# Kernel optimization log

Measured on AMD Instinct MI355X. Metric: run time of the kernel, lower is better.

Reference implementation:

```python
import jax, jax.numpy as jnp
import numpy as np


def setup_inputs() -> dict:
    key = jax.random.key(0)
    k1, k2, k3 = jax.random.split(key, 3)
    T, H, HK, D = 4096, 32, 8, 128  # packed tokens, q heads, kv heads, head dim
    q = jax.random.normal(k1, (T, H, D), dtype=jnp.float32)
    k = jax.random.normal(k2, (T, HK, D), dtype=jnp.float32)
    v = jax.random.normal(k3, (T, HK, D), dtype=jnp.float32)
    return {"q": q, "k": k, "v": v, "num_seqs": 4}


def reference(q, k, v, num_seqs):
    # Varlen prefill causal attention (flash_attn_varlen_func equivalent),
    # equal-length packing: cu_seqlens = [0, S, 2S, ...].
    T, H, D = q.shape
    HK = k.shape[1]
    B = int(num_seqs)
    S = T // B
    scale = 1.0 / jnp.sqrt(jnp.asarray(D, dtype=q.dtype))
    qr = q.reshape(B, S, H, D)
    # GQA: repeat kv heads to match q heads
    rep = H // HK
    kr = jnp.repeat(k.reshape(B, S, HK, D), rep, axis=2)  # [B,S,H,D]
    vr = jnp.repeat(v.reshape(B, S, HK, D), rep, axis=2)
    scores = jnp.einsum("bqhd,bkhd->bhqk", qr, kr) * scale  # [B,H,S,S]
    causal = jnp.tril(jnp.ones((S, S), dtype=bool))
    neg = jnp.asarray(jnp.finfo(scores.dtype).min, dtype=scores.dtype)
    scores = jnp.where(causal, scores, neg)
    p = jax.nn.softmax(scores, axis=-1)
    o = jnp.einsum("bhqk,bkhd->bqhd", p, vr)  # [B,S,H,D]
    return o.reshape(T, H, D)
```

## Files before the change

kernel.cpp:

```cpp
#include <hip/hip_runtime.h>

typedef short short8 __attribute__((ext_vector_type(8)));
typedef float f32x16 __attribute__((ext_vector_type(16)));
typedef int   int4v  __attribute__((ext_vector_type(4)));
typedef int   int2v  __attribute__((ext_vector_type(2)));

#define T_TOK 4096
#define NH    32
#define NKV   8
#define HD    128
#define QREP  (NH / NKV)
#define LDS_PAIR 16384

__device__ __forceinline__ unsigned short f32_to_bf16_bits(float x) {
  union { float f; unsigned u; } a; a.f = x;
  unsigned r = a.u + 0x7fffu + ((a.u >> 16) & 1u);
  return (unsigned short)(r >> 16);
}
__device__ __forceinline__ unsigned pack_bf16(float a, float b) {
  return (unsigned)f32_to_bf16_bits(a) | ((unsigned)f32_to_bf16_bits(b) << 16);
}
__device__ __forceinline__ unsigned cvtpk(float a, float b) {
  unsigned r;
  asm("v_cvt_pk_bf16_f32 %0, %1, %2" : "=v"(r) : "v"(a), "v"(b));
  return r;
}

__device__ __forceinline__ void stage16(const unsigned short* g, unsigned short* l) {
  __builtin_amdgcn_global_load_lds(
      (const __attribute__((address_space(1))) unsigned int*)g,
      (__attribute__((address_space(3))) unsigned int*)l,
      16, 0, 0);
}

__device__ __forceinline__ short8 p_frag(const f32x16& p, int st, int hi) {
  unsigned c01 = cvtpk(p[8*st+0], p[8*st+1]);
  unsigned c23 = cvtpk(p[8*st+2], p[8*st+3]);
  unsigned c45 = cvtpk(p[8*st+4], p[8*st+5]);
  unsigned c67 = cvtpk(p[8*st+6], p[8*st+7]);
  unsigned x01 = (unsigned)__shfl_xor((int)c01, 32, 64);
  unsigned x23 = (unsigned)__shfl_xor((int)c23, 32, 64);
  unsigned x45 = (unsigned)__shfl_xor((int)c45, 32, 64);
  unsigned x67 = (unsigned)__shfl_xor((int)c67, 32, 64);
  int4v pi;
  pi[0] = (int)(hi ? x45 : c01);
  pi[1] = (int)(hi ? x67 : c23);
  pi[2] = (int)(hi ? c45 : x01);
  pi[3] = (int)(hi ? c67 : x23);
  return __builtin_bit_cast(short8, pi);
}

__global__ __launch_bounds__(256)
void pack_k(const float* __restrict__ k, unsigned short* __restrict__ kf,
            const int* __restrict__ nseq) {
  int tid  = blockIdx.x * 256 + threadIdx.x;
  int lane = tid & 63;
  int dc   = (tid >> 6) & 7;
  int gt   = (tid >> 9) & (T_TOK / 32 - 1);
  int kvh  = tid >> 16;
  int c = lane & 31, hi = lane >> 5;
  int token = gt * 32 + c;
  const float* src = k + ((size_t)token * NKV + kvh) * HD + dc * 16 + hi * 8;
  float4 a  = *reinterpret_cast<const float4*>(src);
  float4 b4 = *reinterpret_cast<const float4*>(src + 4);
  const int B = *nseq, S = T_TOK / B, S32 = S >> 5;
  int bseq = gt / S32, tile = gt - bseq * S32;
  size_t off = ((size_t)(bseq * NKV + kvh) * S32 + tile) * 4096 + dc * 512 + lane * 8;
  int4v wv; wv[0] = (int)pack_bf16(a.x, a.y);   wv[1] = (int)pack_bf16(a.z, a.w);
            wv[2] = (int)pack_bf16(b4.x, b4.y); wv[3] = (int)pack_bf16(b4.z, b4.w);
  *reinterpret_cast<int4v*>(kf + off) = wv;
}

__global__ __launch_bounds__(256)
void pack_v(const float* __restrict__ v, unsigned short* __restrict__ vf,
            const int* __restrict__ nseq) {
  int tid  = blockIdx.x * 256 + threadIdx.x;
  int lane = tid & 63;
  int idx  = (tid >> 6) & 7;
  int gt   = (tid >> 9) & (T_TOK / 32 - 1);
  int kvh  = tid >> 16;
  int c = lane & 31, hi = lane >> 5;
  int st = idx >> 2, dt = idx & 3;
  int token0 = gt * 32 + 16 * st + 8 * hi;
  const float* src = v + ((size_t)token0 * NKV + kvh) * HD + dt * 32 + c;
  unsigned u[4];
  #pragma unroll
  for (int jj = 0; jj < 4; ++jj) {
    float a = src[(size_t)(2 * jj)     * (NKV * HD)];
    float b = src[(size_t)(2 * jj + 1) * (NKV * HD)];
    u[jj] = pack_bf16(a, b);
  }
  const int B = *nseq, S = T_TOK / B, S32 = S >> 5;
  int bseq = gt / S32, tile = gt - bseq * S32;
  size_t off = ((size_t)(bseq * NKV + kvh) * S32 + tile) * 4096 + idx * 512 + lane * 8;
  int4v wv; wv[0] = (int)u[0]; wv[1] = (int)u[1]; wv[2] = (int)u[2]; wv[3] = (int)u[3];
  *reinterpret_cast<int4v*>(vf + off) = wv;
}

__global__ __launch_bounds__(256, 2)
void attn_fwd_fast(const float* __restrict__ q,
                   const unsigned short* __restrict__ kfp,
                   const unsigned short* __restrict__ vfp,
                   const int* __restrict__ nseq,
                   float* __restrict__ out)
{
  __shared__ __align__(16) unsigned short sm[2 * LDS_PAIR];

  const int bid  = blockIdx.x;
  const int h    = bid & (NH - 1);
  const int z    = bid >> 5;
  const int w    = threadIdx.x >> 6;
  const int lane = threadIdx.x & 63;
  const int c    = lane & 31;
  const int hi   = lane >> 5;

  const int B = *nseq;
  const int S = T_TOK / B;
  const int S32 = S >> 5;
  const int RBS = S >> 7;

  const int rloc = RBS - 1 - (z / B);
  const int seq  = z - (z / B) * B;
  const int rb   = seq * RBS + rloc;

  const int rbase = rb * 128;
  const int row0  = rbase + w * 32;
  const int s0    = row0 - seq * S;
  const int ntw   = s0 / 32 + 1;
  const int diag  = ntw - 1;
  const int npb   = (rloc * 4 + 4) >> 1;

  const float sl2e = 0.08838834764831845f * 1.4426950408889634f;

  const int kvh = h / QREP;
  const unsigned short* kf_blk = kfp + ((size_t)(seq * NKV + kvh) * S32) * 4096;
  const unsigned short* vf_blk = vfp + ((size_t)(seq * NKV + kvh) * S32) * 4096;
  const unsigned short* sbase = (w & 2) ? vf_blk : kf_blk;

  {
    const unsigned short* src = sbase + (size_t)(w & 1) * 4096 + lane * 8;
    unsigned short* dst = sm + w * 4096;
    #pragma unroll
    for (int j = 0; j < 8; ++j) stage16(src + j * 512, dst + j * 512);
  }

  char* qlds = (char*)(sm + LDS_PAIR);
  {
    #pragma unroll
    for (int j = 0; j < 16; ++j) {
      const int rowb = w * 32 + 2 * j + hi;
      const float* gsrc = q + ((size_t)(rbase + rowb) * NH + h) * HD + 4 * c;
      float4 a = *reinterpret_cast<const float4*>(gsrc);
      int2v u;
      u[0] = (int)cvtpk(a.x * sl2e, a.y * sl2e);
      u[1] = (int)cvtpk(a.z * sl2e, a.w * sl2e);
      const int off = (rowb * 256 + 8 * c) ^ ((rowb & 7) << 4);
      *reinterpret_cast<int2v*>(qlds + off) = u;
    }
  }
  __syncthreads();

  short8 qf[8];
  {
    const int rowb = w * 32 + c;
    #pragma unroll
    for (int dc = 0; dc < 8; ++dc) {
      const int off = (rowb * 256 + dc * 32 + hi * 16) ^ ((c & 7) << 4);
      qf[dc] = *reinterpret_cast<const short8*>(qlds + off);
    }
  }
  __syncthreads();

  f32x16 o0 = {}, o1 = {}, o2 = {}, o3 = {};
  float m = -1e30f, l = 0.0f;

  for (int i = 0; i < npb; ++i) {
    unsigned short* cur = sm + (i & 1) * LDS_PAIR;

    if (i + 1 < npb) {
      const unsigned short* src =
          sbase + (size_t)(2 * (i + 1) + (w & 1)) * 4096 + lane * 8;
      unsigned short* dst = sm + ((i + 1) & 1) * LDS_PAIR + w * 4096;
      #pragma unroll
      for (int j = 0; j < 8; ++j) stage16(src + j * 512, dst + j * 512);
    }

    if (2 * i < ntw) {
      const int ta = 2 * i, tb = 2 * i + 1;
      const unsigned short* kA = cur + lane * 8;
      const unsigned short* kB = cur + 4096 + lane * 8;
      const unsigned short* vA = cur + 8192 + lane * 8;
      const unsigned short* vB = cur + 12288 + lane * 8;

      f32x16 sa = {}, sb = {};
      #pragma unroll
      for (int dc = 0; dc < 8; ++dc) {
        short8 ka  = *reinterpret_cast<const short8*>(kA + dc * 512);
        short8 kb8 = *reinterpret_cast<const short8*>(kB + dc * 512);
        sa = __builtin_amdgcn_mfma_f32_32x32x16_bf16(ka,  qf[dc], sa, 0, 0, 0);
        sb = __builtin_amdgcn_mfma_f32_32x32x16_bf16(kb8, qf[dc], sb, 0, 0, 0);
      }

      const int qs = s0 + c;
      if (tb >= diag) {
        #pragma unroll
        for (int r = 0; r < 16; ++r) {
          int key = tb * 32 + (r & 3) + 8 * (r >> 2) + 4 * hi;
          if (key > qs) sb[r] = -1e30f;
        }
      }
      if (ta >= diag) {
        #pragma unroll
        for (int r = 0; r < 16; ++r) {
          int key = ta * 32 + (r & 3) + 8 * (r >> 2) + 4 * hi;
          if (key > qs) sa[r] = -1e30f;
        }
      }

      float pm = fmaxf(sa[0], sb[0]);
      #pragma unroll
      for (int r = 1; r < 16; ++r) pm = fmaxf(pm, fmaxf(sa[r], sb[r]));
      pm = fmaxf(pm, __shfl_xor(pm, 32));

      if (!__all(pm - m <= 8.0f)) {
        float mn = fmaxf(m, pm);
        float al = __builtin_amdgcn_exp2f(m - mn);
        m = mn;
        l *= al;
        #pragma unroll
        for (int r = 0; r < 16; ++r) {
          float ar = __shfl(al, (r & 3) + 8 * (r >> 2) + 4 * hi, 64);
          o0[r] *= ar; o1[r] *= ar; o2[r] *= ar; o3[r] *= ar;
        }
      }

      float rs = 0.0f;
      f32x16 pA, pB;
      #pragma unroll
      for (int r = 0; r < 16; ++r) {
        pA[r] = __builtin_amdgcn_exp2f(sa[r] - m);
        pB[r] = __builtin_amdgcn_exp2f(sb[r] - m);
        rs += pA[r] + pB[r];
      }
      rs += __shfl_xor(rs, 32);
      l += rs;

      short8 fa0 = p_frag(pA, 0, hi), fa1 = p_frag(pA, 1, hi);
      short8 fb0 = p_frag(pB, 0, hi), fb1 = p_frag(pB, 1, hi);

      short8 va00 = *reinterpret_cast<const short8*>(vA);
      short8 va01 = *reinterpret_cast<const short8*>(vA + 512);
      short8 va02 = *reinterpret_cast<const short8*>(vA + 1024);
      short8 va03 = *reinterpret_cast<const short8*>(vA + 1536);
      short8 va10 = *reinterpret_cast<const short8*>(vA + 2048);
      short8 va11 = *reinterpret_cast<const short8*>(vA + 2560);
      short8 va12 = *reinterpret_cast<const short8*>(vA + 3072);
      short8 va13 = *reinterpret_cast<const short8*>(vA + 3584);
      o0 = __builtin_amdgcn_mfma_f32_32x32x16_bf16(fa0, va00, o0, 0, 0, 0);
      o1 = __builtin_amdgcn_mfma_f32_32x32x16_bf16(fa0, va01, o1, 0, 0, 0);
      o2 = __builtin_amdgcn_mfma_f32_32x32x16_bf16(fa0, va02, o2, 0, 0, 0);
      o3 = __builtin_amdgcn_mfma_f32_32x32x16_bf16(fa0, va03, o3, 0, 0, 0);
      o0 = __builtin_amdgcn_mfma_f32_32x32x16_bf16(fa1, va10, o0, 0, 0, 0);
      o1 = __builtin_amdgcn_mfma_f32_32x32x16_bf16(fa1, va11, o1, 0, 0, 0);
      o2 = __builtin_amdgcn_mfma_f32_32x32x16_bf16(fa1, va12, o2, 0, 0, 0);
      o3 = __builtin_amdgcn_mfma_f32_32x32x16_bf16(fa1, va13, o3, 0, 0, 0);
      short8 vb00 = *reinterpret_cast<const short8*>(vB);
      short8 vb01 = *reinterpret_cast<const short8*>(vB + 512);
      short8 vb02 = *reinterpret_cast<const short8*>(vB + 1024);
      short8 vb03 = *reinterpret_cast<const short8*>(vB + 1536);
      short8 vb10 = *reinterpret_cast<const short8*>(vB + 2048);
      short8 vb11 = *reinterpret_cast<const short8*>(vB + 2560);
      short8 vb12 = *reinterpret_cast<const short8*>(vB + 3072);
      short8 vb13 = *reinterpret_cast<const short8*>(vB + 3584);
      o0 = __builtin_amdgcn_mfma_f32_32x32x16_bf16(fb0, vb00, o0, 0, 0, 0);
      o1 = __builtin_amdgcn_mfma_f32_32x32x16_bf16(fb0, vb01, o1, 0, 0, 0);
      o2 = __builtin_amdgcn_mfma_f32_32x32x16_bf16(fb0, vb02, o2, 0, 0, 0);
      o3 = __builtin_amdgcn_mfma_f32_32x32x16_bf16(fb0, vb03, o3, 0, 0, 0);
      o0 = __builtin_amdgcn_mfma_f32_32x32x16_bf16(fb1, vb10, o0, 0, 0, 0);
      o1 = __builtin_amdgcn_mfma_f32_32x32x16_bf16(fb1, vb11, o1, 0, 0, 0);
      o2 = __builtin_amdgcn_mfma_f32_32x32x16_bf16(fb1, vb12, o2, 0, 0, 0);
      o3 = __builtin_amdgcn_mfma_f32_32x32x16_bf16(fb1, vb13, o3, 0, 0, 0);
    }

    __syncthreads();
  }

  float linv = 1.0f / l;
  #pragma unroll
  for (int r = 0; r < 16; ++r) {
    int qp_ = (r & 3) + 8 * (r >> 2) + 4 * hi;
    float li = __shfl(linv, qp_, 64);
    float* op = out + ((size_t)(row0 + qp_) * NH + h) * HD + c;
    op[0]  = o0[r] * li;
    op[32] = o1[r] * li;
    op[64] = o2[r] * li;
    op[96] = o3[r] * li;
  }
}

__global__ __launch_bounds__(256, 2)
void attn_fwd_slow(const float* __restrict__ q,
                   const float* __restrict__ kp_,
                   const float* __restrict__ vp_,
                   const int* __restrict__ nseq,
                   float* __restrict__ out)
{
  const int bid  = blockIdx.x;
  const int h    = bid & (NH - 1);
  const int rb   = (T_TOK / 128 - 1) - (bid >> 5);
  const int kvh  = h / QREP;
  const int w    = threadIdx.x >> 6;
  const int lane = threadIdx.x & 63;
  const int c    = lane & 31;
  const int hi   = lane >> 5;
  const int B = *nseq, S = T_TOK / B;
  const int row0 = rb * 128 + w * 32;
  const int b = row0 / S, s0 = row0 - b * S, kb = b * S;
  const float sl2e = 0.08838834764831845f * 1.4426950408889634f;
  short8 qf[8];
  {
    const float* qp = q + ((size_t)(row0 + c) * NH + h) * HD + hi * 8;
    #pragma unroll
    for (int dc = 0; dc < 8; ++dc) {
      float4 a  = *reinterpret_cast<const float4*>(qp + dc * 16);
      float4 bq = *reinterpret_cast<const float4*>(qp + dc * 16 + 4);
      int4v wv; wv[0] = (int)pack_bf16(a.x, a.y);   wv[1] = (int)pack_bf16(a.z, a.w);
                wv[2] = (int)pack_bf16(bq.x, bq.y); wv[3] = (int)pack_bf16(bq.z, bq.w);
      qf[dc] = __builtin_bit_cast(short8, wv);
    }
  }
  f32x16 o0 = {}, o1 = {}, o2 = {}, o3 = {};
  float m = -1e30f, l = 0.0f;
  const int ntiles = s0 / 32 + 1;
  for (int t = 0; t < ntiles; ++t) {
    const int key0 = t * 32;
    const size_t koff = ((size_t)(kb + key0 + c) * NKV + kvh) * HD + hi * 8;
    const float* kp = kp_ + koff;
    f32x16 s = {};
    #pragma unroll
    for (int dc = 0; dc < 8; ++dc) {
      float4 a  = *reinterpret_cast<const float4*>(kp + dc * 16);
      float4 bk = *reinterpret_cast<const float4*>(kp + dc * 16 + 4);
      int4v wv; wv[0] = (int)pack_bf16(a.x, a.y);   wv[1] = (int)pack_bf16(a.z, a.w);
                wv[2] = (int)pack_bf16(bk.x, bk.y); wv[3] = (int)pack_bf16(bk.z, bk.w);
      short8 kf = __builtin_bit_cast(short8, wv);
      s = __builtin_amdgcn_mfma_f32_32x32x16_bf16(kf, qf[dc], s, 0, 0, 0);
    }
    if (t == ntiles - 1) {
      const int qs = s0 + c;
      #pragma unroll
      for (int r = 0; r < 16; ++r) {
        int key = key0 + (r & 3) + 8 * (r >> 2) + 4 * hi;
        if (key > qs) s[r] = -1e30f;
      }
    }
    float pm = s[0];
    #pragma unroll
    for (int r = 1; r < 16; ++r) pm = fmaxf(pm, s[r]);
    pm = fmaxf(pm, __shfl_xor(pm, 32));
    if (!__all((pm - m) * sl2e <= 8.0f)) {
      float mn = fmaxf(m, pm);
      float al = __builtin_amdgcn_exp2f(sl2e * (m - mn));
      m = mn; l *= al;
      #pragma unroll
      for (int r = 0; r < 16; ++r) {
        float ar = __shfl(al, (r & 3) + 8 * (r >> 2) + 4 * hi, 64);
        o0[r] *= ar; o1[r] *= ar; o2[r] *= ar; o3[r] *= ar;
      }
    }
    float rs = 0.0f;
    f32x16 p;
    #pragma unroll
    for (int r = 0; r < 16; ++r) {
      p[r] = __builtin_amdgcn_exp2f((s[r] - m) * sl2e);
      rs += p[r];
    }
    rs += __shfl_xor(rs, 32);
    l += rs;
    short8 f0 = p_frag(p, 0, hi), f1 = p_frag(p, 1, hi);
    #pragma unroll
    for (int st = 0; st < 2; ++st) {
      short8 pa = st ? f1 : f0;
      const size_t voff = ((size_t)(kb + key0 + 16*st + 8*hi) * NKV + kvh) * HD + c;
      const float* vp = vp_ + voff;
      float ve[8][4];
      #pragma unroll
      for (int j = 0; j < 8; ++j) {
        const float* vr = vp + (size_t)j * (NKV * HD);
        #pragma unroll
        for (int dt = 0; dt < 4; ++dt) ve[j][dt] = vr[dt * 32];
      }
      #pragma unroll
      for (int dt = 0; dt < 4; ++dt) {
        int4v vb;
        #pragma unroll
        for (int jj = 0; jj < 4; ++jj)
          vb[jj] = (int)pack_bf16(ve[2*jj][dt], ve[2*jj+1][dt]);
        short8 vfx = __builtin_bit_cast(short8, vb);
        if      (dt == 0) o0 = __builtin_amdgcn_mfma_f32_32x32x16_bf16(pa, vfx, o0, 0, 0, 0);
        else if (dt == 1) o1 = __builtin_amdgcn_mfma_f32_32x32x16_bf16(pa, vfx, o1, 0, 0, 0);
        else if (dt == 2) o2 = __builtin_amdgcn_mfma_f32_32x32x16_bf16(pa, vfx, o2, 0, 0, 0);
        else              o3 = __builtin_amdgcn_mfma_f32_32x32x16_bf16(pa, vfx, o3, 0, 0, 0);
      }
    }
  }
  float linv = 1.0f / l;
  #pragma unroll
  for (int r = 0; r < 16; ++r) {
    int qp_ = (r & 3) + 8 * (r >> 2) + 4 * hi;
    float li = __shfl(linv, qp_, 64);
    float* op = out + ((size_t)(row0 + qp_) * NH + h) * HD + c;
    op[0]  = o0[r] * li;
    op[32] = o1[r] * li;
    op[64] = o2[r] * li;
    op[96] = o3[r] * li;
  }
}

extern "C" void kernel_launch(void* const* d_in, const int* in_sizes, int n_in,
                              void* d_out, int out_size, void* d_ws, size_t ws_size,
                              hipStream_t stream) {
  const float* q = (const float*)d_in[0];
  const float* k = (const float*)d_in[1];
  const float* v = (const float*)d_in[2];
  const int* ns  = (const int*)d_in[3];
  float* o       = (float*)d_out;

  const size_t kvElems = (size_t)T_TOK * NKV * HD;
  dim3 grid((T_TOK / 128) * NH);

  if (ws_size >= kvElems * 2 * sizeof(unsigned short)) {
    unsigned short* kfbuf = (unsigned short*)d_ws;
    unsigned short* vfbuf = kfbuf + kvElems;
    pack_k<<<2048, 256, 0, stream>>>(k, kfbuf, ns);
    pack_v<<<2048, 256, 0, stream>>>(v, vfbuf, ns);
    attn_fwd_fast<<<grid, dim3(256), 0, stream>>>(q, kfbuf, vfbuf, ns, o);
  } else {
    attn_fwd_slow<<<grid, dim3(256), 0, stream>>>(q, k, v, ns, o);
  }
}
```

Before: 79.80 us.

## Read V fragments directly from global memory, halve LDS, raise occupancy

Only K tiles are now staged into LDS, double-buffered in half the previous shared memory. V fragments are loaded straight from global memory (through L2) in the layout the MFMA expects. The smaller LDS footprint allows launch bounds of 3 blocks per SM instead of 2, and s_setprio brackets are added around the MFMA runs. The cost is global-load latency on the PV path that is no longer hidden by async LDS staging, plus possible register pressure at the higher occupancy target.

```diff
diff --git a/kernel.cpp b/kernel.cpp
--- a/kernel.cpp
+++ b/kernel.cpp
@@ -10,7 +10,6 @@
 #define NKV   8
 #define HD    128
 #define QREP  (NH / NKV)
-#define LDS_PAIR 16384
 
 __device__ __forceinline__ unsigned short f32_to_bf16_bits(float x) {
   union { float f; unsigned u; } a; a.f = x;
@@ -97,14 +96,14 @@
   *reinterpret_cast<int4v*>(vf + off) = wv;
 }
 
-__global__ __launch_bounds__(256, 2)
+__global__ __launch_bounds__(256, 3)
 void attn_fwd_fast(const float* __restrict__ q,
                    const unsigned short* __restrict__ kfp,
                    const unsigned short* __restrict__ vfp,
                    const int* __restrict__ nseq,
                    float* __restrict__ out)
 {
-  __shared__ __align__(16) unsigned short sm[2 * LDS_PAIR];
+  __shared__ __align__(16) unsigned short sm[16384];
 
   const int bid  = blockIdx.x;
   const int h    = bid & (NH - 1);
@@ -134,17 +133,9 @@
 
   const int kvh = h / QREP;
   const unsigned short* kf_blk = kfp + ((size_t)(seq * NKV + kvh) * S32) * 4096;
-  const unsigned short* vf_blk = vfp + ((size_t)(seq * NKV + kvh) * S32) * 4096;
-  const unsigned short* sbase = (w & 2) ? vf_blk : kf_blk;
-
-  {
-    const unsigned short* src = sbase + (size_t)(w & 1) * 4096 + lane * 8;
-    unsigned short* dst = sm + w * 4096;
-    #pragma unroll
-    for (int j = 0; j < 8; ++j) stage16(src + j * 512, dst + j * 512);
-  }
-
-  char* qlds = (char*)(sm + LDS_PAIR);
+  const unsigned short* vfb = vfp + ((size_t)(seq * NKV + kvh) * S32) * 4096 + lane * 8;
+
+  char* qlds = (char*)sm;
   {
     #pragma unroll
     for (int j = 0; j < 16; ++j) {
@@ -171,28 +162,35 @@
   }
   __syncthreads();
 
+  {
+    const unsigned short* src = kf_blk + (size_t)(w >> 1) * 4096 + (w & 1) * 2048 + lane * 8;
+    unsigned short* dst = sm + w * 2048;
+    #pragma unroll
+    for (int j = 0; j < 4; ++j) stage16(src + j * 512, dst + j * 512);
+  }
+  __syncthreads();
+
   f32x16 o0 = {}, o1 = {}, o2 = {}, o3 = {};
   float m = -1e30f, l = 0.0f;
 
   for (int i = 0; i < npb; ++i) {
-    unsigned short* cur = sm + (i & 1) * LDS_PAIR;
+    const unsigned short* curK = sm + (i & 1) * 8192;
 
     if (i + 1 < npb) {
       const unsigned short* src =
-          sbase + (size_t)(2 * (i + 1) + (w & 1)) * 4096 + lane * 8;
-      unsigned short* dst = sm + ((i + 1) & 1) * LDS_PAIR + w * 4096;
-      #pragma unroll
-      for (int j = 0; j < 8; ++j) stage16(src + j * 512, dst + j * 512);
+          kf_blk + (size_t)(2 * (i + 1) + (w >> 1)) * 4096 + (w & 1) * 2048 + lane * 8;
+      unsigned short* dst = sm + ((i + 1) & 1) * 8192 + w * 2048;
+      #pragma unroll
+      for (int j = 0; j < 4; ++j) stage16(src + j * 512, dst + j * 512);
     }
 
     if (2 * i < ntw) {
       const int ta = 2 * i, tb = 2 * i + 1;
-      const unsigned short* kA = cur + lane * 8;
-      const unsigned short* kB = cur + 4096 + lane * 8;
-      const unsigned short* vA = cur + 8192 + lane * 8;
-      const unsigned short* vB = cur + 12288 + lane * 8;
+      const unsigned short* kA = curK + lane * 8;
+      const unsigned short* kB = curK + 4096 + lane * 8;
 
       f32x16 sa = {}, sb = {};
+      __builtin_amdgcn_s_setprio(1);
       #pragma unroll
       for (int dc = 0; dc < 8; ++dc) {
         short8 ka  = *reinterpret_cast<const short8*>(kA + dc * 512);
@@ -200,6 +198,7 @@
         sa = __builtin_amdgcn_mfma_f32_32x32x16_bf16(ka,  qf[dc], sa, 0, 0, 0);
         sb = __builtin_amdgcn_mfma_f32_32x32x16_bf16(kb8, qf[dc], sb, 0, 0, 0);
       }
+      __builtin_amdgcn_s_setprio(0);
 
       const int qs = s0 + c;
       if (tb >= diag) {
@@ -248,14 +247,17 @@
       short8 fa0 = p_frag(pA, 0, hi), fa1 = p_frag(pA, 1, hi);
       short8 fb0 = p_frag(pB, 0, hi), fb1 = p_frag(pB, 1, hi);
 
-      short8 va00 = *reinterpret_cast<const short8*>(vA);
-      short8 va01 = *reinterpret_cast<const short8*>(vA + 512);
-      short8 va02 = *reinterpret_cast<const short8*>(vA + 1024);
-      short8 va03 = *reinterpret_cast<const short8*>(vA + 1536);
-      short8 va10 = *reinterpret_cast<const short8*>(vA + 2048);
-      short8 va11 = *reinterpret_cast<const short8*>(vA + 2560);
-      short8 va12 = *reinterpret_cast<const short8*>(vA + 3072);
-      short8 va13 = *reinterpret_cast<const short8*>(vA + 3584);
+      const unsigned short* va = vfb + (size_t)ta * 4096;
+      const unsigned short* vb = vfb + (size_t)tb * 4096;
+      short8 va00 = *reinterpret_cast<const short8*>(va);
+      short8 va01 = *reinterpret_cast<const short8*>(va + 512);
+      short8 va02 = *reinterpret_cast<const short8*>(va + 1024);
+      short8 va03 = *reinterpret_cast<const short8*>(va + 1536);
+      short8 va10 = *reinterpret_cast<const short8*>(va + 2048);
+      short8 va11 = *reinterpret_cast<const short8*>(va + 2560);
+      short8 va12 = *reinterpret_cast<const short8*>(va + 3072);
+      short8 va13 = *reinterpret_cast<const short8*>(va + 3584);
+      __builtin_amdgcn_s_setprio(1);
       o0 = __builtin_amdgcn_mfma_f32_32x32x16_bf16(fa0, va00, o0, 0, 0, 0);
       o1 = __builtin_amdgcn_mfma_f32_32x32x16_bf16(fa0, va01, o1, 0, 0, 0);
       o2 = __builtin_amdgcn_mfma_f32_32x32x16_bf16(fa0, va02, o2, 0, 0, 0);
@@ -264,14 +266,16 @@
       o1 = __builtin_amdgcn_mfma_f32_32x32x16_bf16(fa1, va11, o1, 0, 0, 0);
       o2 = __builtin_amdgcn_mfma_f32_32x32x16_bf16(fa1, va12, o2, 0, 0, 0);
       o3 = __builtin_amdgcn_mfma_f32_32x32x16_bf16(fa1, va13, o3, 0, 0, 0);
-      short8 vb00 = *reinterpret_cast<const short8*>(vB);
-      short8 vb01 = *reinterpret_cast<const short8*>(vB + 512);
-      short8 vb02 = *reinterpret_cast<const short8*>(vB + 1024);
-      short8 vb03 = *reinterpret_cast<const short8*>(vB + 1536);
-      short8 vb10 = *reinterpret_cast<const short8*>(vB + 2048);
-      short8 vb11 = *reinterpret_cast<const short8*>(vB + 2560);
-      short8 vb12 = *reinterpret_cast<const short8*>(vB + 3072);
-      short8 vb13 = *reinterpret_cast<const short8*>(vB + 3584);
+      __builtin_amdgcn_s_setprio(0);
+      short8 vb00 = *reinterpret_cast<const short8*>(vb);
+      short8 vb01 = *reinterpret_cast<const short8*>(vb + 512);
+      short8 vb02 = *reinterpret_cast<const short8*>(vb + 1024);
+      short8 vb03 = *reinterpret_cast<const short8*>(vb + 1536);
+      short8 vb10 = *reinterpret_cast<const short8*>(vb + 2048);
+      short8 vb11 = *reinterpret_cast<const short8*>(vb + 2560);
+      short8 vb12 = *reinterpret_cast<const short8*>(vb + 3072);
+      short8 vb13 = *reinterpret_cast<const short8*>(vb + 3584);
+      __builtin_amdgcn_s_setprio(1);
       o0 = __builtin_amdgcn_mfma_f32_32x32x16_bf16(fb0, vb00, o0, 0, 0, 0);
       o1 = __builtin_amdgcn_mfma_f32_32x32x16_bf16(fb0, vb01, o1, 0, 0, 0);
       o2 = __builtin_amdgcn_mfma_f32_32x32x16_bf16(fb0, vb02, o2, 0, 0, 0);
@@ -280,6 +284,7 @@
       o1 = __builtin_amdgcn_mfma_f32_32x32x16_bf16(fb1, vb11, o1, 0, 0, 0);
       o2 = __builtin_amdgcn_mfma_f32_32x32x16_bf16(fb1, vb12, o2, 0, 0, 0);
       o3 = __builtin_amdgcn_mfma_f32_32x32x16_bf16(fb1, vb13, o3, 0, 0, 0);
+      __builtin_amdgcn_s_setprio(0);
     }
 
     __syncthreads();
```

Result: no change. 78.24 us (-1.9%).
